# Performance work log

Measured on AMD Instinct MI355X. Metric: run time of the kernel, lower is better.

## Reference

```python
import jax, jax.numpy as jnp
import numpy as np

BN_EPS = 1e-5


def setup_inputs() -> dict:
    key = jax.random.key(0)
    k1, k2, k3 = jax.random.split(key, 3)
    B, D, L = 8192, 2048, 4  # L = cross_layer + 1
    x = jax.random.normal(k1, (B, D), dtype=jnp.float32)
    w = jax.random.normal(k2, (L, D), dtype=jnp.float32)
    b = jax.random.normal(k3, (L, D), dtype=jnp.float32)
    return {"x": x, "w": w, "b": b}


def reference(x, w, b):
    # x: [B, D]; w, b: [L, D]
    # Original per layer: out = bmm(x0[:, :, None], out[:, None, :]) @ w_l + b_l + out
    # Algebraically identical: out = x0 * (out . w_l) + b_l + out  (associativity)
    # then BatchNorm1d (training, affine=False): normalize with batch mean / biased var.
    x0 = x
    out = x
    n_layers = w.shape[0]  # fixed, small structural loop
    for i in range(n_layers):
        s = jnp.einsum("bd,d->b", out, w[i])          # [B]
        out = x0 * s[:, None] + b[i][None, :] + out    # [B, D]
        mu = jnp.mean(out, axis=0)                     # [D]
        var = jnp.var(out, axis=0)                     # biased variance, [D]
        out = (out - mu) * jax.lax.rsqrt(var + BN_EPS)
    return out
```

## Files before the change

### kernel.cpp

```cpp
#include <hip/hip_runtime.h>
#include <math.h>

#define BB 8192
#define DD 2048
#define BN_EPS 1e-5f
#define NB 512
#define RPB 16
#define PASS_THR 512

#define OFF_T  0
#define OFF_A  (4 * BB)
#define OFF_C  (OFF_A + DD)
#define OFF_E  (OFF_C + 4 * DD)
#define OFF_M1 (OFF_E + DD)
#define OFF_M2 (OFF_M1 + 5 * DD)
#define OFF_MID (OFF_M2 + 15 * DD)
#define OFF_P  (OFF_MID + 16 * 6 * DD)

__host__ __device__ constexpr int P2(int j, int k) { return k * (k + 1) / 2 + j; }

template <int LAY>
__global__ __launch_bounds__(PASS_THR) void k_pass(
    const float* __restrict__ x, const float* __restrict__ w4, float* __restrict__ ws)
{
    constexpr int NV = (LAY == 0) ? 5 : (3 + LAY);
    const float* avec = ws + OFF_A;
    const float* cvec = ws + OFF_C;
    const float* evec = ws + OFF_E;
    float* tbuf     = ws + OFF_T;
    float* partials = ws + OFF_P;

    const int t    = threadIdx.x;
    const int lane = t & 63;
    const int wv   = t >> 6;
    const int blk  = blockIdx.x;
    const int row0 = blk * RPB;
    const int c0   = t * 4;
    const float* wl = w4 + LAY * DD;

    __shared__ float lds_z[8][4][4];
    __shared__ float lds_s[4];
    __shared__ float lds_tv[4][4];
    __shared__ float lds_dote[8];

    float wr[4];
    *(float4*)&wr[0] = *(const float4*)(wl + c0);

    float u0[4], u1[4], u2[4], u3[4];
    if constexpr (LAY == 0) {
        #pragma unroll
        for (int i = 0; i < 4; ++i) u0[i] = wr[i];
    } else {
        float a4[4]; *(float4*)&a4[0] = *(const float4*)(avec + c0);
        #pragma unroll
        for (int i = 0; i < 4; ++i) u0[i] = a4[i] * wr[i];
    }
    if constexpr (LAY >= 1) {
        float cc[4]; *(float4*)&cc[0] = *(const float4*)(cvec + 0 * DD + c0);
        #pragma unroll
        for (int i = 0; i < 4; ++i) u1[i] = cc[i] * wr[i];
    }
    if constexpr (LAY >= 2) {
        float cc[4]; *(float4*)&cc[0] = *(const float4*)(cvec + 1 * DD + c0);
        #pragma unroll
        for (int i = 0; i < 4; ++i) u2[i] = cc[i] * wr[i];
    }
    if constexpr (LAY >= 3) {
        float cc[4]; *(float4*)&cc[0] = *(const float4*)(cvec + 2 * DD + c0);
        #pragma unroll
        for (int i = 0; i < 4; ++i) u3[i] = cc[i] * wr[i];
    }

    float dote = 0.f;
    if constexpr (LAY > 0) {
        float e4[4]; *(float4*)&e4[0] = *(const float4*)(evec + c0);
        float p = e4[0] * wr[0] + e4[1] * wr[1] + e4[2] * wr[2] + e4[3] * wr[3];
        #pragma unroll
        for (int off = 32; off; off >>= 1) p += __shfl_xor(p, off, 64);
        if (lane == 0) lds_dote[wv] = p;
        __syncthreads();
        dote = lds_dote[0] + lds_dote[1] + lds_dote[2] + lds_dote[3]
             + lds_dote[4] + lds_dote[5] + lds_dote[6] + lds_dote[7];
    }

    float pa_m1[4] = {0, 0, 0, 0};
    float pa_20[4] = {0, 0, 0, 0};
    float pa_j1[4] = {0, 0, 0, 0};
    float pa_j2[4] = {0, 0, 0, 0};
    float pa_j3[4] = {0, 0, 0, 0};
    float pa_nn[4] = {0, 0, 0, 0};
    float pa_X1[4] = {0, 0, 0, 0};
    float pa_X2[4] = {0, 0, 0, 0};

    #pragma unroll
    for (int g = 0; g < RPB / 4; ++g) {
        float xr[4][4];
        float zp[4][4];
        #pragma unroll
        for (int rr = 0; rr < 4; ++rr) {
            const int row = row0 + g * 4 + rr;
            *(float4*)&xr[rr][0] = *(const float4*)(x + (size_t)row * DD + c0);
            zp[rr][0] = xr[rr][0] * u0[0] + xr[rr][1] * u0[1]
                      + xr[rr][2] * u0[2] + xr[rr][3] * u0[3];
            if constexpr (LAY >= 1)
                zp[rr][1] = xr[rr][0] * u1[0] + xr[rr][1] * u1[1]
                          + xr[rr][2] * u1[2] + xr[rr][3] * u1[3];
            if constexpr (LAY >= 2)
                zp[rr][2] = xr[rr][0] * u2[0] + xr[rr][1] * u2[1]
                          + xr[rr][2] * u2[2] + xr[rr][3] * u2[3];
            if constexpr (LAY >= 3)
                zp[rr][3] = xr[rr][0] * u3[0] + xr[rr][1] * u3[1]
                          + xr[rr][2] * u3[2] + xr[rr][3] * u3[3];
        }
        #pragma unroll
        for (int off = 32; off; off >>= 1) {
            #pragma unroll
            for (int rr = 0; rr < 4; ++rr) {
                zp[rr][0] += __shfl_xor(zp[rr][0], off, 64);
                if constexpr (LAY >= 1) zp[rr][1] += __shfl_xor(zp[rr][1], off, 64);
                if constexpr (LAY >= 2) zp[rr][2] += __shfl_xor(zp[rr][2], off, 64);
                if constexpr (LAY >= 3) zp[rr][3] += __shfl_xor(zp[rr][3], off, 64);
            }
        }
        if (lane == 0) {
            #pragma unroll
            for (int rr = 0; rr < 4; ++rr) {
                lds_z[wv][rr][0] = zp[rr][0];
                if constexpr (LAY >= 1) lds_z[wv][rr][1] = zp[rr][1];
                if constexpr (LAY >= 2) lds_z[wv][rr][2] = zp[rr][2];
                if constexpr (LAY >= 3) lds_z[wv][rr][3] = zp[rr][3];
            }
        }
        __syncthreads();
        if (t < 4) {
            const int row = row0 + g * 4 + t;
            float z[4] = {0, 0, 0, 0};
            #pragma unroll
            for (int w = 0; w < 8; ++w) {
                z[0] += lds_z[w][t][0];
                if constexpr (LAY >= 1) z[1] += lds_z[w][t][1];
                if constexpr (LAY >= 2) z[2] += lds_z[w][t][2];
                if constexpr (LAY >= 3) z[3] += lds_z[w][t][3];
            }
            float s = z[0] + dote;
            if constexpr (LAY >= 1) {
                const float tv = tbuf[0 * BB + row];
                lds_tv[t][0] = tv; s += tv * z[1];
            }
            if constexpr (LAY >= 2) {
                const float tv = tbuf[1 * BB + row];
                lds_tv[t][1] = tv; s += tv * z[2];
            }
            if constexpr (LAY >= 3) {
                const float tv = tbuf[2 * BB + row];
                lds_tv[t][2] = tv; s += tv * z[3];
            }
            tbuf[LAY * BB + row] = s;
            lds_s[t] = s;
        }
        __syncthreads();
        #pragma unroll
        for (int rr = 0; rr < 4; ++rr) {
            const float s = lds_s[rr];
            #pragma unroll
            for (int i = 0; i < 4; ++i) {
                const float xa = xr[rr][i];
                const float x2 = xa * xa;
                pa_m1[i] = fmaf(xa, s, pa_m1[i]);
                pa_20[i] = fmaf(x2, s, pa_20[i]);
                if constexpr (LAY >= 1) pa_j1[i] = fmaf(x2 * s, lds_tv[rr][0], pa_j1[i]);
                if constexpr (LAY >= 2) pa_j2[i] = fmaf(x2 * s, lds_tv[rr][1], pa_j2[i]);
                if constexpr (LAY >= 3) pa_j3[i] = fmaf(x2 * s, lds_tv[rr][2], pa_j3[i]);
                pa_nn[i] = fmaf(x2 * s, s, pa_nn[i]);
                if constexpr (LAY == 0) {
                    pa_X1[i] += xa;
                    pa_X2[i] += x2;
                }
            }
        }
    }

    float* pp = partials + (size_t)blk * NV * DD + c0;
    *(float4*)(pp + 0 * DD) = *(float4*)&pa_m1[0];
    *(float4*)(pp + 1 * DD) = *(float4*)&pa_20[0];
    if constexpr (LAY == 0) {
        *(float4*)(pp + 2 * DD) = *(float4*)&pa_nn[0];
        *(float4*)(pp + 3 * DD) = *(float4*)&pa_X1[0];
        *(float4*)(pp + 4 * DD) = *(float4*)&pa_X2[0];
    } else {
        if constexpr (LAY >= 1) *(float4*)(pp + 2 * DD) = *(float4*)&pa_j1[0];
        if constexpr (LAY >= 2) *(float4*)(pp + 3 * DD) = *(float4*)&pa_j2[0];
        if constexpr (LAY >= 3) *(float4*)(pp + 4 * DD) = *(float4*)&pa_j3[0];
        *(float4*)(pp + (2 + LAY) * DD) = *(float4*)&pa_nn[0];
    }
}

__global__ __launch_bounds__(256) void k_red_a(
    const float* __restrict__ partials, float* __restrict__ mid,
    int nv, int nchunks)
{
    const int pg = blockIdx.x / nchunks;
    const int ec = blockIdx.x - pg * nchunks;
    const int e  = ec * 256 + threadIdx.x;
    const int p0 = pg * (NB / 16);
    float acc = 0.f;
    #pragma unroll 4
    for (int p = 0; p < NB / 16; ++p)
        acc += partials[(size_t)(p0 + p) * nv * DD + e];
    mid[(size_t)pg * nv * DD + e] = acc;
}

template <int LAY>
__global__ __launch_bounds__(256) void k_stats(float* __restrict__ ws,
                                               const float* __restrict__ b4)
{
    constexpr int NV = (LAY == 0) ? 5 : (3 + LAY);
    const int d = blockIdx.x * 256 + threadIdx.x;
    constexpr int L = LAY + 1;
    float* M1 = ws + OFF_M1;
    float* M2 = ws + OFF_M2;
    const float* mid = ws + OFF_MID;
    float* a = ws + OFF_A;
    float* c = ws + OFF_C;
    float* e = ws + OFF_E;
    const float invB = 1.f / (float)BB;

    float Mn[NV];
    #pragma unroll
    for (int v = 0; v < NV; ++v) {
        float acc = 0.f;
        #pragma unroll
        for (int pg = 0; pg < 16; ++pg)
            acc += mid[(size_t)pg * NV * DD + v * DD + d];
        Mn[v] = acc;
    }

    float g[5], m1v[5], m2v[5][5];

    g[0] = (LAY == 0) ? 1.f : a[d];
    #pragma unroll
    for (int k = 1; k <= LAY; ++k) g[k] = c[(k - 1) * DD + d];
    g[L] = 1.f;

    if constexpr (LAY == 0) m1v[0] = Mn[3];
    else                    m1v[0] = M1[0 * DD + d];
    #pragma unroll
    for (int k = 1; k <= LAY; ++k) m1v[k] = M1[k * DD + d];
    m1v[L] = Mn[0];

    if constexpr (LAY == 0) {
        m2v[0][0] = Mn[4];
    } else {
        #pragma unroll
        for (int k = 0; k <= LAY; ++k)
            #pragma unroll
            for (int j = 0; j <= LAY; ++j)
                if (j <= k) m2v[j][k] = M2[P2(j, k) * DD + d];
    }
    m2v[0][L] = Mn[1];
    #pragma unroll
    for (int j = 1; j <= LAY; ++j) m2v[j][L] = Mn[1 + j];
    m2v[L][L] = Mn[2 + LAY];

    M1[L * DD + d]         = m1v[L];
    M2[P2(0, L) * DD + d]  = m2v[0][L];
    #pragma unroll
    for (int j = 1; j <= LAY; ++j) M2[P2(j, L) * DD + d] = m2v[j][L];
    M2[P2(L, L) * DD + d]  = m2v[L][L];
    if constexpr (LAY == 0) { M1[0 * DD + d] = m1v[0]; M2[0 * DD + d] = m2v[0][0]; }

    const float E = ((LAY == 0) ? 0.f : e[d]) + b4[LAY * DD + d];
    float mxG = 0.f;
    #pragma unroll
    for (int k = 0; k <= L; ++k) mxG += g[k] * m1v[k];
    mxG *= invB;
    const float mu = mxG + E;
    float ex2 = 0.f;
    #pragma unroll
    for (int k = 0; k <= L; ++k) {
        ex2 += g[k] * g[k] * m2v[k][k];
        #pragma unroll
        for (int j = 0; j <= L; ++j)
            if (j < k) ex2 += 2.f * g[j] * g[k] * m2v[j][k];
    }
    ex2 *= invB;
    const float second = ex2 + 2.f * E * mxG + E * E;
    const float var = fmaxf(second - mu * mu, 0.f);
    const float inv = rsqrtf(var + BN_EPS);

    a[d] = g[0] * inv;
    #pragma unroll
    for (int k = 1; k <= LAY; ++k) c[(k - 1) * DD + d] = g[k] * inv;
    c[(L - 1) * DD + d] = inv;
    e[d] = (E - mu) * inv;
}

__global__ __launch_bounds__(256) void k_final(
    const float* __restrict__ x, const float* __restrict__ ws, float* __restrict__ out)
{
    const int t = threadIdx.x;
    const int blk = blockIdx.x;
    const int row0 = blk * 8;
    const int c0 = t * 8;
    const float* a = ws + OFF_A;
    const float* c = ws + OFF_C;
    const float* e = ws + OFF_E;
    const float* tbuf = ws + OFF_T;

    __shared__ float lt[4][8];
    if (t < 32) lt[t >> 3][t & 7] = tbuf[(t >> 3) * BB + row0 + (t & 7)];
    __syncthreads();

    float a8[8], e8[8], c8[4][8];
    *(float4*)&a8[0] = *(const float4*)(a + c0);
    *(float4*)&a8[4] = *(const float4*)(a + c0 + 4);
    *(float4*)&e8[0] = *(const float4*)(e + c0);
    *(float4*)&e8[4] = *(const float4*)(e + c0 + 4);
    #pragma unroll
    for (int k = 0; k < 4; ++k) {
        *(float4*)&c8[k][0] = *(const float4*)(c + k * DD + c0);
        *(float4*)&c8[k][4] = *(const float4*)(c + k * DD + c0 + 4);
    }
    #pragma unroll
    for (int r = 0; r < 8; ++r) {
        const size_t base = (size_t)(row0 + r) * DD + c0;
        float xv[8], o[8];
        *(float4*)&xv[0] = *(const float4*)(x + base);
        *(float4*)&xv[4] = *(const float4*)(x + base + 4);
        const float t0 = lt[0][r], t1 = lt[1][r], t2 = lt[2][r], t3 = lt[3][r];
        #pragma unroll
        for (int i = 0; i < 8; ++i) {
            float gg = a8[i];
            gg = fmaf(c8[0][i], t0, gg);
            gg = fmaf(c8[1][i], t1, gg);
            gg = fmaf(c8[2][i], t2, gg);
            gg = fmaf(c8[3][i], t3, gg);
            o[i] = fmaf(xv[i], gg, e8[i]);
        }
        *(float4*)(out + base)     = *(float4*)&o[0];
        *(float4*)(out + base + 4) = *(float4*)&o[4];
    }
}

extern "C" void kernel_launch(void* const* d_in, const int* in_sizes, int n_in,
                              void* d_out, int out_size, void* d_ws, size_t ws_size,
                              hipStream_t stream) {
    const float* x  = (const float*)d_in[0];
    const float* w  = (const float*)d_in[1];
    const float* bb = (const float*)d_in[2];
    float* out = (float*)d_out;
    float* ws  = (float*)d_ws;
    float* partials = ws + OFF_P;
    float* mid      = ws + OFF_MID;

    k_pass<0><<<NB, PASS_THR, 0, stream>>>(x, w, ws);
    k_red_a<<<16 * 5 * 8, 256, 0, stream>>>(partials, mid, 5, 5 * 8);
    k_stats<0><<<8, 256, 0, stream>>>(ws, bb);

    k_pass<1><<<NB, PASS_THR, 0, stream>>>(x, w, ws);
    k_red_a<<<16 * 4 * 8, 256, 0, stream>>>(partials, mid, 4, 4 * 8);
    k_stats<1><<<8, 256, 0, stream>>>(ws, bb);

    k_pass<2><<<NB, PASS_THR, 0, stream>>>(x, w, ws);
    k_red_a<<<16 * 5 * 8, 256, 0, stream>>>(partials, mid, 5, 5 * 8);
    k_stats<2><<<8, 256, 0, stream>>>(ws, bb);

    k_pass<3><<<NB, PASS_THR, 0, stream>>>(x, w, ws);
    k_red_a<<<16 * 6 * 8, 256, 0, stream>>>(partials, mid, 6, 6 * 8);
    k_stats<3><<<8, 256, 0, stream>>>(ws, bb);

    k_final<<<BB / 8, 256, 0, stream>>>(x, ws, out);
}
```

Measured before the change: 154.0 us.

## Fold per-row t coefficients into weights to use one reduction per row

The per-row tbuf coefficients now scale the u1..u3 vectors before the dot product. Each row then needs one wave shuffle reduction and one LDS slot, instead of up to four separate reductions combined afterwards. The block's tbuf values are preloaded into LDS once, and rows are processed in groups of 8 instead of 4, which halves the barrier count. This costs a few extra FMAs per element and more live registers for the larger x tile, which could lower occupancy.

```diff
diff --git a/kernel.cpp b/kernel.cpp
--- a/kernel.cpp
+++ b/kernel.cpp
@@ -38,9 +38,9 @@
     const int c0   = t * 4;
     const float* wl = w4 + LAY * DD;
 
-    __shared__ float lds_z[8][4][4];
-    __shared__ float lds_s[4];
-    __shared__ float lds_tv[4][4];
+    __shared__ float lds_z[8][8];
+    __shared__ float lds_s[8];
+    __shared__ float lds_t[RPB][4];
     __shared__ float lds_dote[8];
 
     float wr[4];
@@ -69,6 +69,14 @@
         float cc[4]; *(float4*)&cc[0] = *(const float4*)(cvec + 2 * DD + c0);
         #pragma unroll
         for (int i = 0; i < 4; ++i) u3[i] = cc[i] * wr[i];
+    }
+
+    if constexpr (LAY >= 1) {
+        if (t < RPB) {
+            lds_t[t][0] = tbuf[0 * BB + row0 + t];
+            if constexpr (LAY >= 2) lds_t[t][1] = tbuf[1 * BB + row0 + t];
+            if constexpr (LAY >= 3) lds_t[t][2] = tbuf[2 * BB + row0 + t];
+        }
     }
 
     float dote = 0.f;
@@ -93,85 +101,71 @@
     float pa_X2[4] = {0, 0, 0, 0};
 
     #pragma unroll
-    for (int g = 0; g < RPB / 4; ++g) {
-        float xr[4][4];
-        float zp[4][4];
-        #pragma unroll
-        for (int rr = 0; rr < 4; ++rr) {
-            const int row = row0 + g * 4 + rr;
+    for (int g = 0; g < RPB / 8; ++g) {
+        float xr[8][4];
+        float cp[8];
+        #pragma unroll
+        for (int rr = 0; rr < 8; ++rr) {
+            const int row = row0 + g * 8 + rr;
             *(float4*)&xr[rr][0] = *(const float4*)(x + (size_t)row * DD + c0);
-            zp[rr][0] = xr[rr][0] * u0[0] + xr[rr][1] * u0[1]
-                      + xr[rr][2] * u0[2] + xr[rr][3] * u0[3];
-            if constexpr (LAY >= 1)
-                zp[rr][1] = xr[rr][0] * u1[0] + xr[rr][1] * u1[1]
-                          + xr[rr][2] * u1[2] + xr[rr][3] * u1[3];
-            if constexpr (LAY >= 2)
-                zp[rr][2] = xr[rr][0] * u2[0] + xr[rr][1] * u2[1]
-                          + xr[rr][2] * u2[2] + xr[rr][3] * u2[3];
-            if constexpr (LAY >= 3)
-                zp[rr][3] = xr[rr][0] * u3[0] + xr[rr][1] * u3[1]
-                          + xr[rr][2] * u3[2] + xr[rr][3] * u3[3];
-        }
-        #pragma unroll
-        for (int off = 32; off; off >>= 1) {
-            #pragma unroll
-            for (int rr = 0; rr < 4; ++rr) {
-                zp[rr][0] += __shfl_xor(zp[rr][0], off, 64);
-                if constexpr (LAY >= 1) zp[rr][1] += __shfl_xor(zp[rr][1], off, 64);
-                if constexpr (LAY >= 2) zp[rr][2] += __shfl_xor(zp[rr][2], off, 64);
-                if constexpr (LAY >= 3) zp[rr][3] += __shfl_xor(zp[rr][3], off, 64);
-            }
-        }
-        if (lane == 0) {
-            #pragma unroll
-            for (int rr = 0; rr < 4; ++rr) {
-                lds_z[wv][rr][0] = zp[rr][0];
-                if constexpr (LAY >= 1) lds_z[wv][rr][1] = zp[rr][1];
-                if constexpr (LAY >= 2) lds_z[wv][rr][2] = zp[rr][2];
-                if constexpr (LAY >= 3) lds_z[wv][rr][3] = zp[rr][3];
-            }
-        }
-        __syncthreads();
-        if (t < 4) {
-            const int row = row0 + g * 4 + t;
-            float z[4] = {0, 0, 0, 0};
-            #pragma unroll
-            for (int w = 0; w < 8; ++w) {
-                z[0] += lds_z[w][t][0];
-                if constexpr (LAY >= 1) z[1] += lds_z[w][t][1];
-                if constexpr (LAY >= 2) z[2] += lds_z[w][t][2];
-                if constexpr (LAY >= 3) z[3] += lds_z[w][t][3];
-            }
-            float s = z[0] + dote;
+            float we[4];
+            #pragma unroll
+            for (int i = 0; i < 4; ++i) we[i] = u0[i];
             if constexpr (LAY >= 1) {
-                const float tv = tbuf[0 * BB + row];
-                lds_tv[t][0] = tv; s += tv * z[1];
+                const float t1 = lds_t[g * 8 + rr][0];
+                #pragma unroll
+                for (int i = 0; i < 4; ++i) we[i] = fmaf(t1, u1[i], we[i]);
             }
             if constexpr (LAY >= 2) {
-                const float tv = tbuf[1 * BB + row];
-                lds_tv[t][1] = tv; s += tv * z[2];
+                const float t2 = lds_t[g * 8 + rr][1];
+                #pragma unroll
+                for (int i = 0; i < 4; ++i) we[i] = fmaf(t2, u2[i], we[i]);
             }
             if constexpr (LAY >= 3) {
-                const float tv = tbuf[2 * BB + row];
-                lds_tv[t][2] = tv; s += tv * z[3];
+                const float t3 = lds_t[g * 8 + rr][2];
+                #pragma unroll
+                for (int i = 0; i < 4; ++i) we[i] = fmaf(t3, u3[i], we[i]);
             }
+            float a = xr[rr][0] * we[0];
+            a = fmaf(xr[rr][1], we[1], a);
+            a = fmaf(xr[rr][2], we[2], a);
+            a = fmaf(xr[rr][3], we[3], a);
+            cp[rr] = a;
+        }
+        #pragma unroll
+        for (int off = 32; off; off >>= 1) {
+            #pragma unroll
+            for (int rr = 0; rr < 8; ++rr)
+                cp[rr] += __shfl_xor(cp[rr], off, 64);
+        }
+        if (lane == 0) {
+            #pragma unroll
+            for (int rr = 0; rr < 8; ++rr) lds_z[wv][rr] = cp[rr];
+        }
+        __syncthreads();
+        if (t < 8) {
+            const int row = row0 + g * 8 + t;
+            float s = dote;
+            #pragma unroll
+            for (int w = 0; w < 8; ++w) s += lds_z[w][t];
             tbuf[LAY * BB + row] = s;
             lds_s[t] = s;
         }
         __syncthreads();
         #pragma unroll
-        for (int rr = 0; rr < 4; ++rr) {
+        for (int rr = 0; rr < 8; ++rr) {
             const float s = lds_s[rr];
             #pragma unroll
             for (int i = 0; i < 4; ++i) {
                 const float xa = xr[rr][i];
                 const float x2 = xa * xa;
+                const float xs2 = x2 * s;
                 pa_m1[i] = fmaf(xa, s, pa_m1[i]);
-                pa_20[i] = fmaf(x2, s, pa_20[i]);
-                if constexpr (LAY >= 1) pa_j1[i] = fmaf(x2 * s, lds_tv[rr][0], pa_j1[i]);
-                if constexpr (LAY >= 2) pa_j2[i] = fmaf(x2 * s, lds_tv[rr][1], pa_j2[i]);
-                if constexpr (LAY >= 3) pa_j3[i] = fmaf(x2 * s, lds_tv[rr][2], pa_j3[i]);
-                pa_nn[i] = fmaf(x2 * s, s, pa_nn[i]);
+                pa_20[i] += xs2;
+                if constexpr (LAY >= 1) pa_j1[i] = fmaf(xs2, lds_t[g * 8 + rr][0], pa_j1[i]);
+                if constexpr (LAY >= 2) pa_j2[i] = fmaf(xs2, lds_t[g * 8 + rr][1], pa_j2[i]);
+                if constexpr (LAY >= 3) pa_j3[i] = fmaf(xs2, lds_t[g * 8 + rr][2], pa_j3[i]);
+                pa_nn[i] = fmaf(xs2, s, pa_nn[i]);
                 if constexpr (LAY == 0) {
                     pa_X1[i] += xa;
                     pa_X2[i] += x2;
```

Measured after the change: 134.6 us (median of 2 runs). -12.6%, faster.
